# Performance work log

Hardware: AMD Instinct MI355X
Metric: run time of the kernel (lower is better)

The kernel has to match this reference:

```python
import jax, jax.numpy as jnp
import numpy as np

DIM, HEADS, LAYERS, HID = 1024, 16, 6, 4096
PAST_CTX, MAX_PERIOD = 1000, 10000.0
HEAD_DIM = DIM // HEADS


def _ln(x, g, b, eps=1e-5):
    m = jnp.mean(x, axis=-1, keepdims=True)
    v = jnp.mean((x - m) ** 2, axis=-1, keepdims=True)
    return (x - m) * jax.lax.rsqrt(v + eps) * g + b


def setup_inputs() -> dict:
    key = jax.random.key(0)
    ks = jax.random.split(key, 8)
    s = 0.02
    inp = {
        "x": jax.random.normal(ks[0], (2, 2048, DIM), jnp.float32),
        "norm_in_g": jnp.ones((DIM,), jnp.float32),
        "norm_in_b": jnp.zeros((DIM,), jnp.float32),
        "Wqkv": jax.random.normal(ks[1], (LAYERS, 3 * DIM, DIM), jnp.float32) * s,
        "bqkv": jnp.zeros((LAYERS, 3 * DIM), jnp.float32),
        "Wo": jax.random.normal(ks[2], (LAYERS, DIM, DIM), jnp.float32) * s,
        "bo": jnp.zeros((LAYERS, DIM), jnp.float32),
        "ln1_g": jnp.ones((LAYERS, DIM), jnp.float32),
        "ln1_b": jnp.zeros((LAYERS, DIM), jnp.float32),
        "ln2_g": jnp.ones((LAYERS, DIM), jnp.float32),
        "ln2_b": jnp.zeros((LAYERS, DIM), jnp.float32),
        "W1": jax.random.normal(ks[3], (LAYERS, HID, DIM), jnp.float32) * s,
        "b1": jnp.zeros((LAYERS, HID), jnp.float32),
        "W2": jax.random.normal(ks[4], (LAYERS, DIM, HID), jnp.float32) * s,
        "b2": jnp.zeros((LAYERS, DIM), jnp.float32),
    }
    return inp


def _forward(x, norm_in_g, norm_in_b, Wqkv, bqkv, Wo, bo, ln1_g, ln1_b, ln2_g, ln2_b, W1, b1, W2, b2):
    B, T, C = x.shape
    H = 1  # states=None -> per-layer zero cache of length 1
    # sinusoidal positional embedding (offset=0)
    half = C // 2
    positions = jnp.arange(T, dtype=jnp.float32)[None, :, None]  # [1,T,1]
    adim = jnp.arange(half, dtype=jnp.float32)[None, None, :]
    phase = positions / (MAX_PERIOD ** (adim / (half - 1)))
    pos_emb = jnp.concatenate([jnp.cos(phase), jnp.sin(phase)], axis=-1)  # [1,T,C]
    x = _ln(x, norm_in_g, norm_in_b) + pos_emb

    # sliding-window causal mask over keys [past(H) | current(T)]
    q_pos = jnp.arange(H, T + H)[:, None]
    k_pos = jnp.arange(T + H)[None, :]
    delta = q_pos - k_pos
    valid = (delta >= 0) & (delta <= PAST_CTX)  # [T, T+H]
    neg = jnp.finfo(x.dtype).min

    past = jnp.zeros((B, H, C), x.dtype)
    for l in range(LAYERS):
        # post-norm layer (norm_first=False)
        keys = jnp.concatenate([past, x], axis=1)  # [B,T+H,C]
        Wq, Wk, Wv = Wqkv[l][:C], Wqkv[l][C:2 * C], Wqkv[l][2 * C:]
        bq, bk, bv = bqkv[l][:C], bqkv[l][C:2 * C], bqkv[l][2 * C:]
        q = (x @ Wq.T + bq).reshape(B, T, HEADS, HEAD_DIM)
        k = (keys @ Wk.T + bk).reshape(B, T + H, HEADS, HEAD_DIM)
        v = (keys @ Wv.T + bv).reshape(B, T + H, HEADS, HEAD_DIM)
        scores = jnp.einsum('bqhd,bkhd->bhqk', q, k) / jnp.sqrt(jnp.asarray(HEAD_DIM, x.dtype))
        scores = jnp.where(valid[None, None], scores, neg)
        attn = jax.nn.softmax(scores, axis=-1)
        o = jnp.einsum('bhqk,bkhd->bqhd', attn, v).reshape(B, T, C)
        o = o @ Wo[l].T + bo[l]
        x = _ln(x + o, ln1_g[l], ln1_b[l])
        ff = jax.nn.gelu(x @ W1[l].T + b1[l], approximate=False) @ W2[l].T + b2[l]
        x = _ln(x + ff, ln2_g[l], ln2_b[l])
    return x


def reference(x, norm_in_g, norm_in_b, Wqkv, bqkv, Wo, bo, ln1_g, ln1_b, ln2_g, ln2_b, W1, b1, W2, b2):
    return _forward(x, norm_in_g, norm_in_b, Wqkv, bqkv, Wo, bo, ln1_g, ln1_b, ln2_g, ln2_b, W1, b1, W2, b2)
```

## Files before the change

kernel.cpp:

```cpp
#include <hip/hip_runtime.h>
#include <math.h>

typedef short short8 __attribute__((ext_vector_type(8)));
typedef float floatx4 __attribute__((ext_vector_type(4)));

__device__ __forceinline__ unsigned short f2bf(float f) {
  unsigned int u = __builtin_bit_cast(unsigned int, f);
  u = (u + 0x7FFFu + ((u >> 16) & 1u)) >> 16;
  return (unsigned short)u;
}

__device__ __forceinline__ unsigned int pack_bf2(float lo, float hi) {
  return (unsigned int)f2bf(lo) | ((unsigned int)f2bf(hi) << 16);
}

__device__ __forceinline__ void async16(const void* g, void* l) {
  __builtin_amdgcn_global_load_lds(
      (const __attribute__((address_space(1))) unsigned int*)g,
      (__attribute__((address_space(3))) unsigned int*)l, 16, 0, 0);
}

template <int EPI, int TM>
__global__ __launch_bounds__(256, 2) void gemm_bt(
    const unsigned short* __restrict__ A, const unsigned short* __restrict__ B,
    const float* __restrict__ bias, void* __restrict__ outp,
    int M, int N, int K) {
  __shared__ unsigned short As[TM * 32], Bs[4096];
  const int tid = threadIdx.x;
  const int lane = tid & 63;
  const int wid = tid >> 6;
  const int quad = lane >> 4, l15 = lane & 15;
  const int NI = 4, NJ = (TM == 128) ? 4 : 2;
  const int wm = (TM == 128) ? (wid >> 1) : 0;
  const int wn = (TM == 128) ? (wid & 1) : wid;
  const int nwoff = (TM == 128) ? wn * 64 : wn * 32;
  const size_t m0 = (size_t)blockIdx.y * TM, n0 = (size_t)blockIdx.x * 128;
  const int ar = tid >> 2, ak = (tid & 3) * 8;

  floatx4 acc[4][4] = {};

  for (int k0 = 0; k0 < K; k0 += 32) {
    __syncthreads();
    if (TM == 128) {
#pragma unroll
      for (int r = 0; r < 2; ++r) {
        int row = r * 64 + ar;
        async16(A + (m0 + row) * (size_t)K + k0 + ak, &As[(r * 256 + tid) * 8]);
        async16(B + (n0 + row) * (size_t)K + k0 + ak, &Bs[(r * 256 + tid) * 8]);
      }
    } else {
      async16(A + (m0 + ar) * (size_t)K + k0 + ak, &As[tid * 8]);
#pragma unroll
      for (int r = 0; r < 2; ++r) {
        int row = r * 64 + ar;
        async16(B + (n0 + row) * (size_t)K + k0 + ak, &Bs[(r * 256 + tid) * 8]);
      }
    }
    __syncthreads();
    short8 a[4], b[4];
#pragma unroll
    for (int i = 0; i < NI; ++i)
      a[i] = *(const short8*)&As[(wm * 64 + i * 16 + l15) * 32 + quad * 8];
#pragma unroll
    for (int j = 0; j < NJ; ++j)
      b[j] = *(const short8*)&Bs[(nwoff + j * 16 + l15) * 32 + quad * 8];
#pragma unroll
    for (int i = 0; i < NI; ++i)
#pragma unroll
      for (int j = 0; j < NJ; ++j)
        acc[i][j] = __builtin_amdgcn_mfma_f32_16x16x32_bf16(a[i], b[j], acc[i][j], 0, 0, 0);
  }

#pragma unroll
  for (int j = 0; j < NJ; ++j) {
    const int n = (int)n0 + nwoff + j * 16 + l15;
    const float bv = bias[n];
    const float sc = (EPI == 3 && n < 1024) ? 0.125f : 1.0f;
#pragma unroll
    for (int i = 0; i < NI; ++i) {
      const int mbase = (int)m0 + wm * 64 + i * 16 + quad * 4;
#pragma unroll
      for (int r = 0; r < 4; ++r) {
        float v = acc[i][j][r] + bv;
        if (EPI == 2) v = 0.5f * v * (1.0f + erff(v * 0.70710678f));
        if (EPI == 3) v *= sc;
        size_t idx = (size_t)(mbase + r) * (size_t)N + n;
        if (EPI == 1) ((float*)outp)[idx] = v;
        else ((unsigned short*)outp)[idx] = f2bf(v);
      }
    }
  }
}

__global__ __launch_bounds__(512) void attn_kernel(
    const unsigned short* __restrict__ qkv, const float* __restrict__ bqkv_l,
    unsigned short* __restrict__ attno) {
  __shared__ unsigned short Qs[128 * 64];
  __shared__ unsigned short Ks[64 * 64];
  __shared__ unsigned short Vt[64 * 72];
  __shared__ unsigned short Ps[8][16 * 72];
  __shared__ float Lsh[8][16];

  const int qt = blockIdx.x, h = blockIdx.y, b = blockIdx.z;
  const int qs = qt * 128;
  const int tid = threadIdx.x, lane = tid & 63, wid = tid >> 6;
  const int quad = lane >> 4, l15 = lane & 15;
  const size_t rowbase = (size_t)b * 2048;
  const int hoff = h * 64;

#pragma unroll
  for (int r = 0; r < 2; ++r) {
    int c = r * 512 + tid;
    int qrow = c >> 3, ccq = c & 7;
    async16(qkv + (rowbase + qs + qrow) * 3072 + hoff + ccq * 8, &Qs[c * 8]);
  }

  floatx4 oacc[4] = {};
  float lpart = 0.f;

  int kstart = qs - 999;
  if (kstart < 0) kstart = 0;
  kstart &= ~63;
  const int kend = qs + 128;

  const int krow = tid >> 3, cc = tid & 7;
  const int qlo = qs + wid * 16 + 1;
  const int qhi = qlo + 15;
  const int qpos = qs + wid * 16 + l15 + 1;

  for (int k0 = kstart; k0 <= kend; k0 += 64) {
    __syncthreads();
    {
      int xr = k0 + krow - 1;
      xr = xr < 0 ? 0 : (xr > 2047 ? 2047 : xr);
      async16(qkv + (rowbase + xr) * 3072 + 1024 + hoff + cc * 8, &Ks[tid * 8]);
    }
    {
      int xr = k0 + krow - 1;
      xr = xr < 0 ? 0 : (xr > 2047 ? 2047 : xr);
      short8 vv = *(const short8*)(qkv + (rowbase + xr) * 3072 + 2048 + hoff + cc * 8);
#pragma unroll
      for (int e = 0; e < 8; ++e) {
        int e2 = (e + cc) & 7;
        Vt[(cc * 8 + e2) * 72 + krow] = (unsigned short)vv[e2];
      }
    }
    if (k0 == 0) {
      __syncthreads();
      if (tid < 64) {
        Ks[tid] = f2bf(bqkv_l[1024 + hoff + tid]);
        Vt[tid * 72] = f2bf(bqkv_l[2048 + hoff + tid]);
      }
    }
    __syncthreads();

    if (k0 <= qhi && qlo - (k0 + 63) <= 1000) {
      floatx4 sacc[4] = {};
#pragma unroll
      for (int ks = 0; ks < 2; ++ks) {
        short8 bq = *(const short8*)&Qs[(wid * 16 + l15) * 64 + ks * 32 + quad * 8];
#pragma unroll
        for (int nj = 0; nj < 4; ++nj) {
          short8 ak = *(const short8*)&Ks[(nj * 16 + l15) * 64 + ks * 32 + quad * 8];
          sacc[nj] = __builtin_amdgcn_mfma_f32_16x16x32_bf16(ak, bq, sacc[nj], 0, 0, 0);
        }
      }

      const bool full = (k0 + 63 <= qlo) && (qhi - k0 <= 1000);
#pragma unroll
      for (int nj = 0; nj < 4; ++nj) {
        float e[4];
        if (full) {
#pragma unroll
          for (int r = 0; r < 4; ++r) e[r] = __expf(sacc[nj][r]);
        } else {
          const int keyb = k0 + nj * 16 + quad * 4;
#pragma unroll
          for (int r = 0; r < 4; ++r) {
            int delta = qpos - (keyb + r);
            e[r] = (delta >= 0 && delta <= 1000) ? __expf(sacc[nj][r]) : 0.f;
          }
        }
        lpart += (e[0] + e[1]) + (e[2] + e[3]);
        uint2 pk = make_uint2(pack_bf2(e[0], e[1]), pack_bf2(e[2], e[3]));
        *(uint2*)&Ps[wid][l15 * 72 + nj * 16 + quad * 4] = pk;
      }

#pragma unroll
      for (int ks = 0; ks < 2; ++ks) {
        short8 pf = *(const short8*)&Ps[wid][l15 * 72 + ks * 32 + quad * 8];
#pragma unroll
        for (int di = 0; di < 4; ++di) {
          short8 vf = *(const short8*)&Vt[(di * 16 + l15) * 72 + ks * 32 + quad * 8];
          oacc[di] = __builtin_amdgcn_mfma_f32_16x16x32_bf16(pf, vf, oacc[di], 0, 0, 0);
        }
      }
    }
  }

  lpart += __shfl_xor(lpart, 16);
  lpart += __shfl_xor(lpart, 32);
  if (quad == 0) Lsh[wid][l15] = lpart;
  __builtin_amdgcn_s_waitcnt(0);
  float linv[4];
#pragma unroll
  for (int r = 0; r < 4; ++r) linv[r] = 1.0f / Lsh[wid][quad * 4 + r];

#pragma unroll
  for (int di = 0; di < 4; ++di)
#pragma unroll
    for (int r = 0; r < 4; ++r) {
      int q = qs + wid * 16 + quad * 4 + r;
      attno[(rowbase + q) * 1024 + hoff + di * 16 + l15] =
          f2bf(oacc[di][r] * linv[r]);
    }
}

__global__ __launch_bounds__(256) void ln_first_kernel(
    const float* __restrict__ xin, const float* __restrict__ g,
    const float* __restrict__ bb, float* __restrict__ xout,
    unsigned short* __restrict__ xbout) {
  const int row = blockIdx.x, tid = threadIdx.x;
  const size_t base = (size_t)row * 1024 + tid * 4;
  float4 xv = *(const float4*)&xin[base];
  float s = xv.x + xv.y + xv.z + xv.w;
  float sq = xv.x * xv.x + xv.y * xv.y + xv.z * xv.z + xv.w * xv.w;
  __shared__ float red[8];
  for (int off = 32; off > 0; off >>= 1) { s += __shfl_down(s, off); sq += __shfl_down(sq, off); }
  if ((tid & 63) == 0) { red[tid >> 6] = s; red[4 + (tid >> 6)] = sq; }
  __syncthreads();
  s = red[0] + red[1] + red[2] + red[3];
  sq = red[4] + red[5] + red[6] + red[7];
  const float mean = s * (1.f / 1024.f);
  const float rstd = rsqrtf(sq * (1.f / 1024.f) - mean * mean + 1e-5f);
  float4 gv = *(const float4*)&g[tid * 4];
  float4 bv = *(const float4*)&bb[tid * 4];
  const float tf = (float)(row & 2047);
  float xs[4] = {xv.x, xv.y, xv.z, xv.w};
  float gs[4] = {gv.x, gv.y, gv.z, gv.w};
  float bs[4] = {bv.x, bv.y, bv.z, bv.w};
  float y[4];
#pragma unroll
  for (int e = 0; e < 4; ++e) {
    int c = tid * 4 + e;
    float a = (c < 512) ? (float)c : (float)(c - 512);
    float ph = tf * powf(10000.f, -a * (1.f / 511.f));
    float pe = (c < 512) ? cosf(ph) : sinf(ph);
    y[e] = (xs[e] - mean) * rstd * gs[e] + bs[e] + pe;
  }
  *(float4*)&xout[base] = make_float4(y[0], y[1], y[2], y[3]);
  *(ushort4*)&xbout[base] = make_ushort4(f2bf(y[0]), f2bf(y[1]), f2bf(y[2]), f2bf(y[3]));
}

__global__ __launch_bounds__(256) void ln_res_kernel(
    const float* __restrict__ xin, const float* __restrict__ addv,
    const float* __restrict__ g, const float* __restrict__ bb,
    float* __restrict__ xout, unsigned short* __restrict__ xbout) {
  const int row = blockIdx.x, tid = threadIdx.x;
  const size_t base = (size_t)row * 1024 + tid * 4;
  float4 xv = *(const float4*)&xin[base];
  float4 av = *(const float4*)&addv[base];
  float v0 = xv.x + av.x, v1 = xv.y + av.y, v2 = xv.z + av.z, v3 = xv.w + av.w;
  float s = v0 + v1 + v2 + v3;
  float sq = v0 * v0 + v1 * v1 + v2 * v2 + v3 * v3;
  __shared__ float red[8];
  for (int off = 32; off > 0; off >>= 1) { s += __shfl_down(s, off); sq += __shfl_down(sq, off); }
  if ((tid & 63) == 0) { red[tid >> 6] = s; red[4 + (tid >> 6)] = sq; }
  __syncthreads();
  s = red[0] + red[1] + red[2] + red[3];
  sq = red[4] + red[5] + red[6] + red[7];
  const float mean = s * (1.f / 1024.f);
  const float rstd = rsqrtf(sq * (1.f / 1024.f) - mean * mean + 1e-5f);
  float4 gv = *(const float4*)&g[tid * 4];
  float4 bv = *(const float4*)&bb[tid * 4];
  float vs[4] = {v0, v1, v2, v3};
  float gs[4] = {gv.x, gv.y, gv.z, gv.w};
  float bs[4] = {bv.x, bv.y, bv.z, bv.w};
  float y[4];
#pragma unroll
  for (int e = 0; e < 4; ++e) y[e] = (vs[e] - mean) * rstd * gs[e] + bs[e];
  *(float4*)&xout[base] = make_float4(y[0], y[1], y[2], y[3]);
  if (xbout)
    *(ushort4*)&xbout[base] = make_ushort4(f2bf(y[0]), f2bf(y[1]), f2bf(y[2]), f2bf(y[3]));
}

__global__ __launch_bounds__(256) void convw_kernel(
    const float* __restrict__ wqkv, const float* __restrict__ wo,
    const float* __restrict__ w1, const float* __restrict__ w2,
    unsigned short* __restrict__ dst) {
  for (int base = blockIdx.x * 256 + threadIdx.x; base < 3145728; base += 786432) {
    int i = base << 2;
    const float* src;
    int off;
    if (i < 3145728)      { src = wqkv; off = i; }
    else if (i < 4194304) { src = wo;   off = i - 3145728; }
    else if (i < 8388608) { src = w1;   off = i - 4194304; }
    else                  { src = w2;   off = i - 8388608; }
    float4 v = *(const float4*)&src[off];
    *(ushort4*)&dst[i] = make_ushort4(f2bf(v.x), f2bf(v.y), f2bf(v.z), f2bf(v.w));
  }
}

extern "C" void kernel_launch(void* const* d_in, const int* in_sizes, int n_in,
                              void* d_out, int out_size, void* d_ws, size_t ws_size,
                              hipStream_t stream) {
  const float* x    = (const float*)d_in[0];
  const float* ng   = (const float*)d_in[1];
  const float* nb   = (const float*)d_in[2];
  const float* Wqkv = (const float*)d_in[3];
  const float* bqkv = (const float*)d_in[4];
  const float* Wo   = (const float*)d_in[5];
  const float* bo   = (const float*)d_in[6];
  const float* ln1g = (const float*)d_in[7];
  const float* ln1b = (const float*)d_in[8];
  const float* ln2g = (const float*)d_in[9];
  const float* ln2b = (const float*)d_in[10];
  const float* W1   = (const float*)d_in[11];
  const float* b1   = (const float*)d_in[12];
  const float* W2   = (const float*)d_in[13];
  const float* b2   = (const float*)d_in[14];

  char* ws = (char*)d_ws;
  float* xf           = (float*)(ws + 0);
  unsigned short* xb  = (unsigned short*)(ws + 16777216);
  unsigned short* qkv = (unsigned short*)(ws + 25165824);
  unsigned short* att = (unsigned short*)(ws + 50331648);
  unsigned short* h1  = (unsigned short*)(ws + 58720256);
  float* gout         = (float*)(ws + 92274688);
  unsigned short* wb  = (unsigned short*)(ws + 109051904);
  unsigned short* wqkvb = wb;
  unsigned short* wob   = wb + 3145728;
  unsigned short* w1b   = wb + 4194304;
  unsigned short* w2b   = wb + 8388608;

  ln_first_kernel<<<4096, 256, 0, stream>>>(x, ng, nb, xf, xb);

  for (int l = 0; l < 6; ++l) {
    convw_kernel<<<3072, 256, 0, stream>>>(Wqkv + (size_t)l * 3145728,
                                           Wo + (size_t)l * 1048576,
                                           W1 + (size_t)l * 4194304,
                                           W2 + (size_t)l * 4194304, wb);
    gemm_bt<3, 128><<<dim3(24, 32), 256, 0, stream>>>(xb, wqkvb, bqkv + l * 3072, qkv,
                                                      4096, 3072, 1024);
    attn_kernel<<<dim3(16, 16, 2), 512, 0, stream>>>(qkv, bqkv + l * 3072, att);
    gemm_bt<1, 64><<<dim3(8, 64), 256, 0, stream>>>(att, wob, bo + l * 1024, gout,
                                                    4096, 1024, 1024);
    ln_res_kernel<<<4096, 256, 0, stream>>>(xf, gout, ln1g + l * 1024, ln1b + l * 1024,
                                            xf, xb);
    gemm_bt<2, 128><<<dim3(32, 32), 256, 0, stream>>>(xb, w1b, b1 + l * 4096, h1,
                                                      4096, 4096, 1024);
    gemm_bt<1, 64><<<dim3(8, 64), 256, 0, stream>>>(h1, w2b, b2 + l * 1024, gout,
                                                    4096, 1024, 4096);
    ln_res_kernel<<<4096, 256, 0, stream>>>(xf, gout, ln2g + l * 1024, ln2b + l * 1024,
                                            (l == 5) ? (float*)d_out : xf,
                                            (l == 5) ? nullptr : xb);
  }
}
```

Baseline: 1.930 ms.

## Triple-buffer GEMM LDS tiles with async prefetch and XOR swizzle

Turns the bf16 MFMA GEMM main loop into a three-stage pipeline: global-to-LDS async loads are issued two K-steps ahead, with explicit vmcnt waits and raw barriers in place of the two __syncthreads per iteration. The LDS layout is XOR-swizzled on the K chunk to cut bank conflicts on fragment reads, and MFMA issue priority is raised with s_setprio. This targets load latency and LDS conflicts in every projection and FFN GEMM, at the cost of tripled LDS use, which may limit occupancy with launch bounds of 2 blocks per CU.

Result: no change. 1.960 ms (+1.5%).

```diff
diff --git a/kernel.cpp b/kernel.cpp
--- a/kernel.cpp
+++ b/kernel.cpp
@@ -25,7 +25,10 @@
     const unsigned short* __restrict__ A, const unsigned short* __restrict__ B,
     const float* __restrict__ bias, void* __restrict__ outp,
     int M, int N, int K) {
-  __shared__ unsigned short As[TM * 32], Bs[4096];
+  constexpr int ABUF = TM * 32;
+  constexpr int NL = (TM == 128) ? 4 : 3;
+  __shared__ unsigned short As[3 * ABUF];
+  __shared__ unsigned short Bs[3 * 4096];
   const int tid = threadIdx.x;
   const int lane = tid & 63;
   const int wid = tid >> 6;
@@ -35,40 +38,75 @@
   const int wn = (TM == 128) ? (wid & 1) : wid;
   const int nwoff = (TM == 128) ? wn * 64 : wn * 32;
   const size_t m0 = (size_t)blockIdx.y * TM, n0 = (size_t)blockIdx.x * 128;
-  const int ar = tid >> 2, ak = (tid & 3) * 8;
+  const int ar = tid >> 2;
+  const int ak = (((tid & 3) ^ ((ar >> 1) & 3)) * 8);
 
   floatx4 acc[4][4] = {};
 
-  for (int k0 = 0; k0 < K; k0 += 32) {
-    __syncthreads();
+  auto stage = [&](int ib, int kk) {
     if (TM == 128) {
 #pragma unroll
       for (int r = 0; r < 2; ++r) {
         int row = r * 64 + ar;
-        async16(A + (m0 + row) * (size_t)K + k0 + ak, &As[(r * 256 + tid) * 8]);
-        async16(B + (n0 + row) * (size_t)K + k0 + ak, &Bs[(r * 256 + tid) * 8]);
+        async16(A + (m0 + row) * (size_t)K + kk + ak,
+                &As[ib * ABUF + (r * 256 + tid) * 8]);
+        async16(B + (n0 + row) * (size_t)K + kk + ak,
+                &Bs[ib * 4096 + (r * 256 + tid) * 8]);
       }
     } else {
-      async16(A + (m0 + ar) * (size_t)K + k0 + ak, &As[tid * 8]);
+      async16(A + (m0 + ar) * (size_t)K + kk + ak, &As[ib * ABUF + tid * 8]);
 #pragma unroll
       for (int r = 0; r < 2; ++r) {
         int row = r * 64 + ar;
-        async16(B + (n0 + row) * (size_t)K + k0 + ak, &Bs[(r * 256 + tid) * 8]);
-      }
-    }
-    __syncthreads();
+        async16(B + (n0 + row) * (size_t)K + kk + ak,
+                &Bs[ib * 4096 + (r * 256 + tid) * 8]);
+      }
+    }
+  };
+
+  stage(0, 0);
+  if (K > 32) stage(1, 32);
+  const int csw = (l15 >> 1) & 3;
+  int ib = 0;
+
+  for (int k0 = 0; k0 < K; k0 += 32) {
+    int ib2 = ib + 2;
+    if (ib2 >= 3) ib2 -= 3;
+    if (k0 + 64 < K) {
+      stage(ib2, k0 + 64);
+      asm volatile("s_waitcnt vmcnt(%0)" ::"n"(2 * NL) : "memory");
+    } else if (k0 + 32 < K) {
+      asm volatile("s_waitcnt vmcnt(%0)" ::"n"(NL) : "memory");
+    } else {
+      asm volatile("s_waitcnt vmcnt(0)" ::: "memory");
+    }
+    __builtin_amdgcn_s_barrier();
+    __builtin_amdgcn_sched_barrier(0);
+
     short8 a[4], b[4];
 #pragma unroll
     for (int i = 0; i < NI; ++i)
-      a[i] = *(const short8*)&As[(wm * 64 + i * 16 + l15) * 32 + quad * 8];
+      a[i] = *(const short8*)&As[ib * ABUF + (wm * 64 + i * 16 + l15) * 32 +
+                                 (quad ^ csw) * 8];
 #pragma unroll
     for (int j = 0; j < NJ; ++j)
-      b[j] = *(const short8*)&Bs[(nwoff + j * 16 + l15) * 32 + quad * 8];
+      b[j] = *(const short8*)&Bs[ib * 4096 + (nwoff + j * 16 + l15) * 32 +
+                                 (quad ^ csw) * 8];
+    asm volatile("s_waitcnt lgkmcnt(0)" ::: "memory");
+    __builtin_amdgcn_sched_barrier(0);
+    __builtin_amdgcn_s_barrier();
+
+    __builtin_amdgcn_s_setprio(1);
 #pragma unroll
     for (int i = 0; i < NI; ++i)
 #pragma unroll
       for (int j = 0; j < NJ; ++j)
-        acc[i][j] = __builtin_amdgcn_mfma_f32_16x16x32_bf16(a[i], b[j], acc[i][j], 0, 0, 0);
+        acc[i][j] = __builtin_amdgcn_mfma_f32_16x16x32_bf16(a[i], b[j],
+                                                            acc[i][j], 0, 0, 0);
+    __builtin_amdgcn_s_setprio(0);
+
+    ib = ib + 1;
+    if (ib >= 3) ib -= 3;
   }
 
 #pragma unroll
```

## Replace GEMM with triple-buffered, swizzled, larger-tile 512-thread kernel

Applied to the files above, without the earlier changes.

Replaces the single-buffered 32-wide-K GEMM with a kernel that stages 64-wide K tiles into three LDS buffers using async global-to-LDS loads. Loads for tile k+2 are issued while tile k is being computed, with explicit vmcnt waits. It also XOR-swizzles the LDS layout to avoid bank conflicts, doubles the block tile to 256 or 128 rows with 8 waves, remaps block IDs to improve L2 reuse, and raises wave priority around the MFMA section. The goal is to hide global-load latency and cut barrier overhead in the GEMMs, which dominate the runtime. In exchange it uses more LDS and registers, which may lower occupancy, and leaves fewer blocks in the grid.

New measurement: 1.752 ms. 9.2% less time.

```diff
diff --git a/kernel.cpp b/kernel.cpp
--- a/kernel.cpp
+++ b/kernel.cpp
@@ -20,65 +20,110 @@
       (__attribute__((address_space(3))) unsigned int*)l, 16, 0, 0);
 }
 
-template <int EPI, int TM>
-__global__ __launch_bounds__(256, 2) void gemm_bt(
+template <int EPI, int BM>
+__global__ __launch_bounds__(512, 2) void gemm3(
     const unsigned short* __restrict__ A, const unsigned short* __restrict__ B,
     const float* __restrict__ bias, void* __restrict__ outp,
     int M, int N, int K) {
-  __shared__ unsigned short As[TM * 32], Bs[4096];
+  constexpr int BN = 128;
+  constexpr int ROWS = BM + BN;
+  constexpr int BUFE = ROWS * 64;
+  constexpr int NLT = ROWS / 64;
+  constexpr int WM = BM / 64;
+  constexpr int WN = 8 / WM;
+  constexpr int NJ = (BN / WN) / 16;
+  __shared__ unsigned short S[3 * BUFE];
+
   const int tid = threadIdx.x;
-  const int lane = tid & 63;
-  const int wid = tid >> 6;
+  const int lane = tid & 63, wid = tid >> 6;
   const int quad = lane >> 4, l15 = lane & 15;
-  const int NI = 4, NJ = (TM == 128) ? 4 : 2;
-  const int wm = (TM == 128) ? (wid >> 1) : 0;
-  const int wn = (TM == 128) ? (wid & 1) : wid;
-  const int nwoff = (TM == 128) ? wn * 64 : wn * 32;
-  const size_t m0 = (size_t)blockIdx.y * TM, n0 = (size_t)blockIdx.x * 128;
-  const int ar = tid >> 2, ak = (tid & 3) * 8;
-
-  floatx4 acc[4][4] = {};
-
-  for (int k0 = 0; k0 < K; k0 += 32) {
-    __syncthreads();
-    if (TM == 128) {
-#pragma unroll
-      for (int r = 0; r < 2; ++r) {
-        int row = r * 64 + ar;
-        async16(A + (m0 + row) * (size_t)K + k0 + ak, &As[(r * 256 + tid) * 8]);
-        async16(B + (n0 + row) * (size_t)K + k0 + ak, &Bs[(r * 256 + tid) * 8]);
-      }
+  const int wm = wid / WN, wn = wid % WN;
+  const int wmo = wm * 64;
+  const int wno = wn * (BN / WN);
+
+  const int gx = gridDim.x;
+  const int nwg = gx * gridDim.y;
+  int lin = blockIdx.y * gx + blockIdx.x;
+  lin = (lin & 7) * (nwg >> 3) + (lin >> 3);
+  const size_t m0 = (size_t)(lin / gx) * BM;
+  const size_t n0 = (size_t)(lin % gx) * BN;
+
+  auto stage = [&](int buf, int kt) {
+#pragma unroll
+    for (int l = 0; l < NLT; ++l) {
+      int ci = l * 512 + tid;
+      int r = ci >> 3;
+      int c = (ci & 7) ^ (r & 7);
+      const unsigned short* src =
+          (r < BM) ? A + (m0 + r) * (size_t)K + kt + c * 8
+                   : B + (n0 + (r - BM)) * (size_t)K + kt + c * 8;
+      async16(src, &S[buf * BUFE + ci * 8]);
+    }
+  };
+
+  floatx4 acc[4][NJ] = {};
+
+  stage(0, 0);
+  stage(1, 64);
+  int cur = 0;
+
+  for (int kt = 0; kt < K; kt += 64) {
+    if (kt + 128 < K) {
+      int nb = cur + 2;
+      if (nb >= 3) nb -= 3;
+      stage(nb, kt + 128);
+      asm volatile("s_waitcnt vmcnt(%0)" ::"n"(2 * NLT) : "memory");
+    } else if (kt + 64 < K) {
+      asm volatile("s_waitcnt vmcnt(%0)" ::"n"(NLT) : "memory");
     } else {
-      async16(A + (m0 + ar) * (size_t)K + k0 + ak, &As[tid * 8]);
-#pragma unroll
-      for (int r = 0; r < 2; ++r) {
-        int row = r * 64 + ar;
-        async16(B + (n0 + row) * (size_t)K + k0 + ak, &Bs[(r * 256 + tid) * 8]);
-      }
-    }
-    __syncthreads();
-    short8 a[4], b[4];
-#pragma unroll
-    for (int i = 0; i < NI; ++i)
-      a[i] = *(const short8*)&As[(wm * 64 + i * 16 + l15) * 32 + quad * 8];
-#pragma unroll
-    for (int j = 0; j < NJ; ++j)
-      b[j] = *(const short8*)&Bs[(nwoff + j * 16 + l15) * 32 + quad * 8];
-#pragma unroll
-    for (int i = 0; i < NI; ++i)
-#pragma unroll
-      for (int j = 0; j < NJ; ++j)
-        acc[i][j] = __builtin_amdgcn_mfma_f32_16x16x32_bf16(a[i], b[j], acc[i][j], 0, 0, 0);
+      asm volatile("s_waitcnt vmcnt(0)" ::: "memory");
+    }
+    __builtin_amdgcn_s_barrier();
+    __builtin_amdgcn_sched_barrier(0);
+
+    short8 a[4][2], b[NJ][2];
+    const unsigned short* Sc = &S[cur * BUFE];
+#pragma unroll
+    for (int i = 0; i < 4; ++i) {
+      const int R = wmo + i * 16 + l15;
+#pragma unroll
+      for (int kh = 0; kh < 2; ++kh)
+        a[i][kh] = *(const short8*)&Sc[R * 64 + (((kh * 4 + quad) ^ (R & 7)) * 8)];
+    }
+#pragma unroll
+    for (int j = 0; j < NJ; ++j) {
+      const int R = BM + wno + j * 16 + l15;
+#pragma unroll
+      for (int kh = 0; kh < 2; ++kh)
+        b[j][kh] = *(const short8*)&Sc[R * 64 + (((kh * 4 + quad) ^ (R & 7)) * 8)];
+    }
+    asm volatile("s_waitcnt lgkmcnt(0)" ::: "memory");
+    __builtin_amdgcn_sched_barrier(0);
+    __builtin_amdgcn_s_barrier();
+
+    __builtin_amdgcn_s_setprio(1);
+#pragma unroll
+    for (int kh = 0; kh < 2; ++kh)
+#pragma unroll
+      for (int i = 0; i < 4; ++i)
+#pragma unroll
+        for (int j = 0; j < NJ; ++j)
+          acc[i][j] = __builtin_amdgcn_mfma_f32_16x16x32_bf16(
+              a[i][kh], b[j][kh], acc[i][j], 0, 0, 0);
+    __builtin_amdgcn_s_setprio(0);
+
+    ++cur;
+    if (cur >= 3) cur -= 3;
   }
 
 #pragma unroll
   for (int j = 0; j < NJ; ++j) {
-    const int n = (int)n0 + nwoff + j * 16 + l15;
+    const int n = (int)n0 + wno + j * 16 + l15;
     const float bv = bias[n];
     const float sc = (EPI == 3 && n < 1024) ? 0.125f : 1.0f;
 #pragma unroll
-    for (int i = 0; i < NI; ++i) {
-      const int mbase = (int)m0 + wm * 64 + i * 16 + quad * 4;
+    for (int i = 0; i < 4; ++i) {
+      const int mbase = (int)m0 + wmo + i * 16 + quad * 4;
 #pragma unroll
       for (int r = 0; r < 4; ++r) {
         float v = acc[i][j][r] + bv;
@@ -340,17 +385,17 @@
                                            Wo + (size_t)l * 1048576,
                                            W1 + (size_t)l * 4194304,
                                            W2 + (size_t)l * 4194304, wb);
-    gemm_bt<3, 128><<<dim3(24, 32), 256, 0, stream>>>(xb, wqkvb, bqkv + l * 3072, qkv,
-                                                      4096, 3072, 1024);
+    gemm3<3, 256><<<dim3(24, 16), 512, 0, stream>>>(xb, wqkvb, bqkv + l * 3072, qkv,
+                                                    4096, 3072, 1024);
     attn_kernel<<<dim3(16, 16, 2), 512, 0, stream>>>(qkv, bqkv + l * 3072, att);
-    gemm_bt<1, 64><<<dim3(8, 64), 256, 0, stream>>>(att, wob, bo + l * 1024, gout,
-                                                    4096, 1024, 1024);
+    gemm3<1, 128><<<dim3(8, 32), 512, 0, stream>>>(att, wob, bo + l * 1024, gout,
+                                                   4096, 1024, 1024);
     ln_res_kernel<<<4096, 256, 0, stream>>>(xf, gout, ln1g + l * 1024, ln1b + l * 1024,
                                             xf, xb);
-    gemm_bt<2, 128><<<dim3(32, 32), 256, 0, stream>>>(xb, w1b, b1 + l * 4096, h1,
-                                                      4096, 4096, 1024);
-    gemm_bt<1, 64><<<dim3(8, 64), 256, 0, stream>>>(h1, w2b, b2 + l * 1024, gout,
-                                                    4096, 1024, 4096);
+    gemm3<2, 256><<<dim3(32, 16), 512, 0, stream>>>(xb, w1b, b1 + l * 4096, h1,
+                                                    4096, 4096, 1024);
+    gemm3<1, 128><<<dim3(8, 32), 512, 0, stream>>>(h1, w2b, b2 + l * 1024, gout,
+                                                   4096, 1024, 4096);
     ln_res_kernel<<<4096, 256, 0, stream>>>(xf, gout, ln2g + l * 1024, ln2b + l * 1024,
                                             (l == 5) ? (float*)d_out : xf,
                                             (l == 5) ? nullptr : xb);
```
